# Optimization experiments

Measured on AMD Instinct MI355X. Metric: run time of the kernel, lower is better.

The kernel has to match this reference:

```python
import itertools
import jax, jax.numpy as jnp
import numpy as np

ALPHA = 1e-4   # mse/conn mixing
BETA = 0.1
DMAX = 20.0
NCAP = 10.0    # costs_n_cap
PCAP = 3.0     # costs_p_cap
W3D = 64       # 3D cube window (window_3d)
W2D = 32       # 2D MALIS window (window_2d, default)


def _dilate5(mask):
    # scipy binary_dilation, default cross structuring element, 5 iterations
    m = mask.astype(bool)
    for _ in range(5):
        p = np.pad(m, 1)
        m = p[1:-1, 1:-1] | p[:-2, 1:-1] | p[2:, 1:-1] | p[1:-1, :-2] | p[1:-1, 2:]
    return m


def _label8(mask):
    # skimage.measure.label on boolean mask: 8-connectivity, background=0
    H, W = mask.shape
    lbl = np.zeros((H, W), np.int64)
    parent = {}

    def find(x):
        while parent[x] != x:
            parent[x] = parent[parent[x]]
            x = parent[x]
        return x

    nxt = 1
    for i in range(H):
        for j in range(W):
            if not mask[i, j]:
                continue
            neigh = []
            for di, dj in ((-1, -1), (-1, 0), (-1, 1), (0, -1)):
                ii, jj = i + di, j + dj
                if 0 <= ii < H and 0 <= jj < W and mask[ii, jj]:
                    neigh.append(int(lbl[ii, jj]))
            if not neigh:
                lbl[i, j] = nxt
                parent[nxt] = nxt
                nxt += 1
            else:
                m0 = min(neigh)
                lbl[i, j] = m0
                for nb in neigh:
                    ra, rb = find(m0), find(nb)
                    if ra != rb:
                        parent[max(ra, rb)] = min(ra, rb)
    out = np.zeros_like(lbl)
    remap = {}
    c = 0
    for i in range(H):
        for j in range(W):
            if lbl[i, j] > 0:
                r = find(int(lbl[i, j]))
                if r not in remap:
                    c += 1
                    remap[r] = c
                out[i, j] = remap[r]
    return out


def _malis_edge_weights(seg, n1, n2, costs, pos):
    # MALIS union-find / Kruskal maximal-spanning-tree pair counting.
    # Edges processed in descending cost order. Background (seg==0) nodes
    # are not counted. pos=1: #same-label pairs merged; pos=0: #diff-label pairs.
    n = seg.size
    parent = list(range(n))

    def find(x):
        r = x
        while parent[r] != r:
            r = parent[r]
        while parent[x] != r:
            parent[x], x = r, parent[x]
        return r

    cnt = [({int(s): 1} if s > 0 else {}) for s in seg]
    tot = [1 if s > 0 else 0 for s in seg]
    w = np.zeros(costs.shape[0], np.float32)
    for e in np.argsort(-costs, kind="stable"):
        ra, rb = find(int(n1[e])), find(int(n2[e]))
        if ra == rb:
            continue
        ca, cb = cnt[ra], cnt[rb]
        if len(ca) > len(cb):
            ra, rb, ca, cb = rb, ra, cb, ca
        same = 0
        for l, v in ca.items():
            same += v * cb.get(l, 0)
        w[e] = float(same if pos else tot[ra] * tot[rb] - same)
        for l, v in ca.items():
            cb[l] = cb.get(l, 0) + v
        tot[rb] += tot[ra]
        parent[ra] = rb
        cnt[ra] = None
    return w


def _window_weights(pred2d, tgt2d):
    # numpy MALIS node weights for a [B,1,H,W] 2D projection
    B, C, H, W = pred2d.shape
    w = W2D
    wn = np.zeros(pred2d.shape, np.float32)
    wp = np.zeros(pred2d.shape, np.float32)
    idx = np.arange(w * w).reshape(w, w)
    n1 = np.concatenate([idx[:, :-1].ravel(), idx[:-1, :].ravel()])
    n2 = np.concatenate([idx[:, 1:].ravel(), idx[1:, :].ravel()])
    nh = w * (w - 1)
    for k in range(H // w):
        for j in range(W // w):
            p = pred2d[:, :, k*w:(k+1)*w, j*w:(j+1)*w]
            t = tgt2d[:, :, k*w:(k+1)*w, j*w:(j+1)*w]
            ch = (p[:, :, :, :-1] + p[:, :, :, 1:]).reshape(B, -1)
            cv = (p[:, :, :-1, :] + p[:, :, 1:, :]).reshape(B, -1)
            costs = np.concatenate([ch, cv], 1).astype(np.float32)
            gh = (t[:, :, :, :-1] + t[:, :, :, 1:]).reshape(B, -1)
            gv = (t[:, :, :-1, :] + t[:, :, 1:, :]).reshape(B, -1)
            gt = np.concatenate([gh, gv], 1).astype(np.float32)
            costs_n = costs.copy()
            costs_p = costs.copy()
            costs_n[gt > NCAP] = NCAP
            costs_p[gt < PCAP] = 0.0
            gt = np.minimum(gt, NCAP)
            for b in range(B):
                sg = _label8(~_dilate5(t[b, 0] == 0)).ravel()
                en = _malis_edge_weights(sg, n1, n2, costs_n[b], 0)
                ep = _malis_edge_weights(sg, n1, n2, costs_p[b], 1)
                sn = en.sum()
                if sn > 0:
                    en = en / sn
                sp = ep.sum()
                if sp > 0:
                    ep = ep / sp
                en[gt[b] >= PCAP] = 0.0
                ep[gt[b] < NCAP] = 0.0
                for ew, out in ((en, wn), (ep, wp)):
                    eh = ew[:nh].reshape(w, w - 1)
                    ev = ew[nh:].reshape(w - 1, w)
                    nwt = np.zeros((w, w), np.float32)
                    nwt[:, :-1] += eh
                    nwt[:, 1:] += eh
                    nwt[:-1, :] += ev
                    nwt[1:, :] += ev
                    out[b, 0, k*w:(k+1)*w, j*w:(j+1)*w] = nwt
    return wn, wp


def _precompute(pred_np, tgt_np):
    # host-side (detached) MALIS weight maps, exactly as the torch module
    B, C, H, W, D = pred_np.shape
    items = []
    for k, j, i in itertools.product(range(H // W3D), range(W // W3D), range(D // W3D)):
        sl = (slice(None), slice(None), slice(k*W3D, (k+1)*W3D),
              slice(j*W3D, (j+1)*W3D), slice(i*W3D, (i+1)*W3D))
        pc, tc = pred_np[sl], tgt_np[sl]
        for axis in (2, 3, 4):
            wn, wp = _window_weights(pc.min(axis=axis), tc.min(axis=axis))
            items.append((k, j, i, axis, jnp.asarray(wn), jnp.asarray(wp)))
    return items


def _loss(pred, target, items):
    mse = jnp.mean((pred - target) ** 2)
    conn = jnp.float32(0.0)
    for (k, j, i, axis, wn, wp) in items:
        pc = pred[:, :, k*W3D:(k+1)*W3D, j*W3D:(j+1)*W3D, i*W3D:(i+1)*W3D]
        proj = jnp.min(pc, axis=axis)  # [B,1,64,64]
        conn = conn + jnp.sum(proj**2 * wn + BETA * (DMAX - proj)**2 * wp)
    return (mse, jnp.float32(ALPHA) * conn)


def setup_inputs() -> dict:
    # synthetic distance-transform-like volumes (zeros on 'vessel' seeds)
    rng = np.random.default_rng(0)
    B, H = 4, 128
    g = np.arange(H, dtype=np.float32)
    zz, yy, xx = np.meshgrid(g, g, g, indexing="ij")
    tgt = np.empty((B, 1, H, H, H), np.float32)
    for b in range(B):
        pts = rng.uniform(0, H, size=(24, 3)).astype(np.float32)
        d = np.full((H, H, H), np.inf, np.float32)
        for p in pts:
            d = np.minimum(d, np.sqrt((zz - p[0])**2 + (yy - p[1])**2 + (xx - p[2])**2))
        tgt[b, 0] = np.floor(np.minimum(d, DMAX))
    pred = np.clip(tgt + 0.5 * rng.standard_normal(tgt.shape).astype(np.float32), 0.0, DMAX).astype(np.float32)
    return {"pred": jnp.asarray(pred), "target": jnp.asarray(tgt)}


def reference(pred, target):
    items = _precompute(np.asarray(pred), np.asarray(target))
    return _loss(pred, target, items)
```

## Files before the change

kernel.cpp:

```cpp
#include <hip/hip_runtime.h>

#define BLOCK 256
#define NNODE 1024
#define NH    992
#define NE    1984
#define NSORT 2048
#define LMAX  12
#define CHUNK 64
#define NPASS (NE / CHUNK)

typedef unsigned long long ull;

__device__ __forceinline__ void edge_nodes(int e, int& a, int& b) {
    if (e < NH) {
        int r = e / 31;
        int c = e - r * 31;
        a = (r << 5) + c;
        b = a + 1;
    } else {
        a = e - NH;
        b = a + 32;
    }
}

__device__ __forceinline__ int find_par(unsigned short* par, int x) {
    volatile unsigned short* vp = par;
    int r = x;
    int p = vp[r];
    while (p != r) { r = p; p = vp[r]; }
    int c = x;
    while (c != r) { const int nxt = vp[c]; vp[c] = (unsigned short)r; c = nxt; }
    return r;
}

__device__ __forceinline__ int dot16x4(ull a, ull b) {
    int s  = (int)(a & 0xFFFFu)         * (int)(b & 0xFFFFu);
    s     += (int)((a >> 16) & 0xFFFFu) * (int)((b >> 16) & 0xFFFFu);
    s     += (int)((a >> 32) & 0xFFFFu) * (int)((b >> 32) & 0xFFFFu);
    s     += (int)((a >> 48) & 0xFFFFu) * (int)((b >> 48) & 0xFFFFu);
    return s;
}

__device__ __forceinline__ void cswap(unsigned int& ka, unsigned short& ia,
                                      unsigned int& kb, unsigned short& ib, bool up) {
    const bool gt = (ka > kb) || (ka == kb && ia > ib);
    if (gt == up) {
        const unsigned int  tk = ka; ka = kb; kb = tk;
        const unsigned short ti = ia; ia = ib; ib = ti;
    }
}

__global__ __launch_bounds__(BLOCK) void conn_kernel(const float* __restrict__ pred,
                                                     const float* __restrict__ tgt,
                                                     double* __restrict__ acc_ws,
                                                     int B) {
    __shared__ alignas(16) float          sh_p[NNODE];
    __shared__ alignas(16) float          sh_t[NNODE];
    __shared__ alignas(16) unsigned int   sh_key[NSORT];
    __shared__ alignas(16) unsigned short sh_idx[NSORT];
    __shared__ unsigned short sh_parent[NNODE];
    __shared__ unsigned int   sh_szto[NNODE];
    __shared__ ull            sh_cnt64[NNODE * 3];
    __shared__ unsigned char  sh_seg[NNODE];
    __shared__ int            sh_flag;
    __shared__ int            sh_L;
    __shared__ float          sh_sn;
    __shared__ double         sh_red[4];

    const int tid = threadIdx.x;
    int wg = blockIdx.x;
    const int sign = (wg >> 3) & 1;
    wg = (wg & 7) | ((wg >> 4) << 3);
    const int b    = wg % B;  wg /= B;
    const int win  = wg & 3;  wg >>= 2;
    const int item = wg;
    const int axis_id = item % 3;
    const int cube = item / 3;
    const int ci = cube & 1;
    const int cj = (cube >> 1) & 1;
    const int ck = (cube >> 2) & 1;
    const int wk = win >> 1;
    const int wj = win & 1;

    const size_t base = (size_t)b * 2097152u;

    if (axis_id == 2) {
        for (int pix = tid; pix < NNODE; pix += BLOCK) {
            const int r = pix >> 5, c = pix & 31;
            const int R = wk * 32 + r, C = wj * 32 + c;
            const size_t idx0 = base + (size_t)(ck * 64 + R) * 16384u + (size_t)(cj * 64 + C) * 128u + (size_t)(ci * 64);
            const float4* pp = reinterpret_cast<const float4*>(pred + idx0);
            const float4* tp = reinterpret_cast<const float4*>(tgt + idx0);
            float pm = 3.4e38f, tm = 3.4e38f;
            #pragma unroll
            for (int h = 0; h < 16; ++h) {
                const float4 a = pp[h];
                const float4 t = tp[h];
                pm = fminf(pm, fminf(fminf(a.x, a.y), fminf(a.z, a.w)));
                tm = fminf(tm, fminf(fminf(t.x, t.y), fminf(t.z, t.w)));
            }
            sh_p[pix] = pm;
            sh_t[pix] = tm;
        }
    } else {
        const int r  = tid >> 3;
        const int c0 = (tid & 7) << 2;
        const int R = wk * 32 + r, C = wj * 32 + c0;
        size_t idx0; int hstride;
        if (axis_id == 0) {
            idx0 = base + (size_t)(ck * 64) * 16384u + (size_t)(cj * 64 + R) * 128u + (size_t)(ci * 64 + C);
            hstride = 16384;
        } else {
            idx0 = base + (size_t)(ck * 64 + R) * 16384u + (size_t)(cj * 64) * 128u + (size_t)(ci * 64 + C);
            hstride = 128;
        }
        float4 pm = make_float4(3.4e38f, 3.4e38f, 3.4e38f, 3.4e38f);
        float4 tm = pm;
        #pragma unroll 8
        for (int h = 0; h < 64; ++h) {
            const float4 a  = *reinterpret_cast<const float4*>(pred + idx0);
            const float4 t4 = *reinterpret_cast<const float4*>(tgt + idx0);
            pm.x = fminf(pm.x, a.x);  pm.y = fminf(pm.y, a.y);
            pm.z = fminf(pm.z, a.z);  pm.w = fminf(pm.w, a.w);
            tm.x = fminf(tm.x, t4.x); tm.y = fminf(tm.y, t4.y);
            tm.z = fminf(tm.z, t4.z); tm.w = fminf(tm.w, t4.w);
            idx0 += (size_t)hstride;
        }
        *reinterpret_cast<float4*>(&sh_p[(r << 5) + c0]) = pm;
        *reinterpret_cast<float4*>(&sh_t[(r << 5) + c0]) = tm;
    }
    __syncthreads();

    unsigned char* mA = sh_seg;
    unsigned char* mB = (unsigned char*)sh_idx;
    for (int pix = tid; pix < NNODE; pix += BLOCK)
        mA[pix] = (sh_t[pix] == 0.0f) ? 1 : 0;
    __syncthreads();
    for (int it = 0; it < 5; ++it) {
        unsigned char* src = (it & 1) ? mB : mA;
        unsigned char* dst = (it & 1) ? mA : mB;
        for (int pix = tid; pix < NNODE; pix += BLOCK) {
            const int r = pix >> 5, c = pix & 31;
            unsigned char v = src[pix];
            if (r > 0)  v |= src[pix - 32];
            if (r < 31) v |= src[pix + 32];
            if (c > 0)  v |= src[pix - 1];
            if (c < 31) v |= src[pix + 1];
            dst[pix] = v;
        }
        __syncthreads();
    }
    for (int pix = tid; pix < NNODE; pix += BLOCK)
        mA[pix] = mB[pix] ^ 1;
    __syncthreads();

    for (int pix = tid; pix < NNODE; pix += BLOCK)
        sh_parent[pix] = mA[pix] ? (unsigned short)pix : (unsigned short)0xFFFF;
    __syncthreads();
    for (;;) {
        if (tid == 0) sh_flag = 0;
        __syncthreads();
        for (int pix = tid; pix < NNODE; pix += BLOCK) {
            if (!mA[pix]) continue;
            const int r = pix >> 5, c = pix & 31;
            int m = sh_parent[pix];
            #pragma unroll
            for (int d = 0; d < 8; ++d) {
                static const int dr[8] = {-1,-1,-1, 0, 0, 1, 1, 1};
                static const int dc[8] = {-1, 0, 1,-1, 1,-1, 0, 1};
                const int rr = r + dr[d], cc = c + dc[d];
                if (rr < 0 || rr > 31 || cc < 0 || cc > 31) continue;
                const int nb = (rr << 5) + cc;
                if (mA[nb]) { int v = sh_parent[nb]; if (v < m) m = v; }
            }
            while ((int)sh_parent[m] < m) m = sh_parent[m];
            if (m < (int)sh_parent[pix]) { sh_parent[pix] = (unsigned short)m; sh_flag = 1; }
        }
        __syncthreads();
        const int f = sh_flag;
        __syncthreads();
        if (f == 0) break;
    }

    if (tid == 0) sh_L = 0;
    __syncthreads();
    for (int pix = tid; pix < NNODE; pix += BLOCK) {
        if (mA[pix] && (int)sh_parent[pix] == pix) {
            const int id = atomicAdd(&sh_L, 1);
            sh_szto[pix] = (unsigned int)(id + 1);
        }
    }
    __syncthreads();
    for (int pix = tid; pix < NNODE; pix += BLOCK) {
        unsigned char s = 0;
        if (mA[pix]) {
            int lab = (int)sh_szto[sh_parent[pix]];
            if (lab > 255) lab = 255;
            s = (unsigned char)lab;
        }
        sh_seg[pix] = s;
    }
    __syncthreads();

    const int Lraw = sh_L;
    const int mode = (Lraw <= 1) ? 0 : ((Lraw <= 4) ? 1 : 2);
    const bool skip_all = (Lraw == 0) || (Lraw == 1 && sign == 0);

    if (!skip_all) {

    for (int pix = tid; pix < NNODE; pix += BLOCK) {
        sh_parent[pix] = (unsigned short)pix;
        const int s = sh_seg[pix];
        const unsigned int tot = (s > 0 && s <= LMAX) ? 1u : 0u;
        sh_szto[pix] = 1u | (tot << 16);
        if (mode >= 1) {
            ull c0 = 0, c1 = 0, c2 = 0;
            if (s >= 1 && s <= LMAX) {
                const ull bit = 1ull << (((s - 1) & 3) * 16);
                const int q = (s - 1) >> 2;
                if (q == 0) c0 = bit; else if (q == 1) c1 = bit; else c2 = bit;
            }
            sh_cnt64[pix * 3 + 0] = c0;
            if (mode == 2) {
                sh_cnt64[pix * 3 + 1] = c1;
                sh_cnt64[pix * 3 + 2] = c2;
            }
        }
    }
    __syncthreads();

    unsigned int   K[8];
    unsigned short I[8];
    const int b8 = tid << 3;
    #pragma unroll
    for (int l = 0; l < 8; ++l) {
        const int e = b8 + l;
        if (e < NE) {
            int a, bb; edge_nodes(e, a, bb);
            float cost = sh_p[a] + sh_p[bb];
            const float g = sh_t[a] + sh_t[bb];
            if (sign == 0) { if (g > 10.0f) cost = 10.0f; }
            else           { if (g <  3.0f) cost = 0.0f;  }
            K[l] = ~__float_as_uint(cost);
            I[l] = (unsigned short)e;
        } else {
            K[l] = 0xFFFFFFFFu;
            I[l] = (unsigned short)0xFFFF;
        }
    }
    cswap(K[0],I[0],K[1],I[1], true );
    cswap(K[2],I[2],K[3],I[3], false);
    cswap(K[4],I[4],K[5],I[5], true );
    cswap(K[6],I[6],K[7],I[7], false);
    cswap(K[0],I[0],K[2],I[2], true );
    cswap(K[1],I[1],K[3],I[3], true );
    cswap(K[4],I[4],K[6],I[6], false);
    cswap(K[5],I[5],K[7],I[7], false);
    cswap(K[0],I[0],K[1],I[1], true );
    cswap(K[2],I[2],K[3],I[3], true );
    cswap(K[4],I[4],K[5],I[5], false);
    cswap(K[6],I[6],K[7],I[7], false);
    {
        const bool u8 = ((b8 & 8) == 0);
        cswap(K[0],I[0],K[4],I[4], u8); cswap(K[1],I[1],K[5],I[5], u8);
        cswap(K[2],I[2],K[6],I[6], u8); cswap(K[3],I[3],K[7],I[7], u8);
        cswap(K[0],I[0],K[2],I[2], u8); cswap(K[1],I[1],K[3],I[3], u8);
        cswap(K[4],I[4],K[6],I[6], u8); cswap(K[5],I[5],K[7],I[7], u8);
        cswap(K[0],I[0],K[1],I[1], u8); cswap(K[2],I[2],K[3],I[3], u8);
        cswap(K[4],I[4],K[5],I[5], u8); cswap(K[6],I[6],K[7],I[7], u8);
    }
    {
        uint4 k0, k1, iv;
        k0.x=K[0]; k0.y=K[1]; k0.z=K[2]; k0.w=K[3];
        k1.x=K[4]; k1.y=K[5]; k1.z=K[6]; k1.w=K[7];
        iv.x=(unsigned int)I[0] | ((unsigned int)I[1]<<16);
        iv.y=(unsigned int)I[2] | ((unsigned int)I[3]<<16);
        iv.z=(unsigned int)I[4] | ((unsigned int)I[5]<<16);
        iv.w=(unsigned int)I[6] | ((unsigned int)I[7]<<16);
        *reinterpret_cast<uint4*>(&sh_key[b8])     = k0;
        *reinterpret_cast<uint4*>(&sh_key[b8 + 4]) = k1;
        *reinterpret_cast<uint4*>(&sh_idx[b8])     = iv;
    }
    __syncthreads();

    for (int k = 16; k <= NSORT; k <<= 1) {
        for (int j = k >> 1; j >= 8; j >>= 1) {
            for (int p = tid; p < (NSORT >> 1); p += BLOCK) {
                const int i   = ((p & ~(j - 1)) << 1) | (p & (j - 1));
                const int ixj = i | j;
                const unsigned int ka = sh_key[i], kb = sh_key[ixj];
                const unsigned short ia = sh_idx[i], ib = sh_idx[ixj];
                const bool gt = (ka > kb) || (ka == kb && ia > ib);
                const bool up = ((i & k) == 0);
                if (gt == up) {
                    sh_key[i] = kb; sh_key[ixj] = ka;
                    sh_idx[i] = ib; sh_idx[ixj] = ia;
                }
            }
            __syncthreads();
        }
        {
            const uint4 k0 = *reinterpret_cast<const uint4*>(&sh_key[b8]);
            const uint4 k1 = *reinterpret_cast<const uint4*>(&sh_key[b8 + 4]);
            const uint4 iv = *reinterpret_cast<const uint4*>(&sh_idx[b8]);
            K[0]=k0.x; K[1]=k0.y; K[2]=k0.z; K[3]=k0.w;
            K[4]=k1.x; K[5]=k1.y; K[6]=k1.z; K[7]=k1.w;
            I[0]=(unsigned short)(iv.x); I[1]=(unsigned short)(iv.x>>16);
            I[2]=(unsigned short)(iv.y); I[3]=(unsigned short)(iv.y>>16);
            I[4]=(unsigned short)(iv.z); I[5]=(unsigned short)(iv.z>>16);
            I[6]=(unsigned short)(iv.w); I[7]=(unsigned short)(iv.w>>16);
            const bool u8 = ((b8 & k) == 0);
            cswap(K[0],I[0],K[4],I[4], u8); cswap(K[1],I[1],K[5],I[5], u8);
            cswap(K[2],I[2],K[6],I[6], u8); cswap(K[3],I[3],K[7],I[7], u8);
            cswap(K[0],I[0],K[2],I[2], u8); cswap(K[1],I[1],K[3],I[3], u8);
            cswap(K[4],I[4],K[6],I[6], u8); cswap(K[5],I[5],K[7],I[7], u8);
            cswap(K[0],I[0],K[1],I[1], u8); cswap(K[2],I[2],K[3],I[3], u8);
            cswap(K[4],I[4],K[5],I[5], u8); cswap(K[6],I[6],K[7],I[7], u8);
            uint4 o0, o1, ov;
            o0.x=K[0]; o0.y=K[1]; o0.z=K[2]; o0.w=K[3];
            o1.x=K[4]; o1.y=K[5]; o1.z=K[6]; o1.w=K[7];
            ov.x=(unsigned int)I[0] | ((unsigned int)I[1]<<16);
            ov.y=(unsigned int)I[2] | ((unsigned int)I[3]<<16);
            ov.z=(unsigned int)I[4] | ((unsigned int)I[5]<<16);
            ov.w=(unsigned int)I[6] | ((unsigned int)I[7]<<16);
            *reinterpret_cast<uint4*>(&sh_key[b8])     = o0;
            *reinterpret_cast<uint4*>(&sh_key[b8 + 4]) = o1;
            *reinterpret_cast<uint4*>(&sh_idx[b8])     = ov;
        }
        __syncthreads();
    }

    for (int e = tid; e < NE; e += BLOCK) sh_key[e] = 0u;
    __syncthreads();

    if (tid < 64) {
        const int lane = tid;
        for (int pass = 0; pass < NPASS; ++pass) {
            const int e = sh_idx[pass * CHUNK + lane];
            int a, bb; edge_nodes(e, a, bb);
            int ra = find_par(sh_parent, a);
            int rb = find_par(sh_parent, bb);
            ull m = __ballot(ra != rb);
            while (m) {
                const int i = (int)__builtin_ctzll(m);
                m &= m - 1;
                const unsigned int pack = (unsigned int)ra | ((unsigned int)rb << 10) | ((unsigned int)e << 20);
                const unsigned int pk = (unsigned int)__shfl((int)pack, i);
                const int ra_i = (int)(pk & 1023u);
                const int rb_i = (int)((pk >> 10) & 1023u);
                if (ra_i == rb_i) continue;
                const int se = (int)(pk >> 20);
                const unsigned int xa = sh_szto[ra_i], xb = sh_szto[rb_i];
                const int ta = (int)(xa >> 16), tb = (int)(xb >> 16);
                const int big = ((xa & 0xFFFFu) > (xb & 0xFFFFu));
                const int rs = big ? ra_i : rb_i;
                const int rl = big ? rb_i : ra_i;
                int wv;
                if (mode == 0) {
                    wv = ta * tb;
                } else if (mode == 1) {
                    const ull a0 = sh_cnt64[ra_i * 3];
                    const ull b0 = sh_cnt64[rb_i * 3];
                    const int same = dot16x4(a0, b0);
                    wv = sign ? same : (ta * tb - same);
                    if (lane == 0 && (ta + tb) > 0)
                        sh_cnt64[rs * 3] = a0 + b0;
                } else {
                    const ull a0 = sh_cnt64[ra_i * 3 + 0];
                    const ull a1 = sh_cnt64[ra_i * 3 + 1];
                    const ull a2 = sh_cnt64[ra_i * 3 + 2];
                    const ull b0 = sh_cnt64[rb_i * 3 + 0];
                    const ull b1 = sh_cnt64[rb_i * 3 + 1];
                    const ull b2 = sh_cnt64[rb_i * 3 + 2];
                    const int same = dot16x4(a0, b0) + dot16x4(a1, b1) + dot16x4(a2, b2);
                    wv = sign ? same : (ta * tb - same);
                    if (lane == 0 && (ta + tb) > 0) {
                        sh_cnt64[rs * 3 + 0] = a0 + b0;
                        sh_cnt64[rs * 3 + 1] = a1 + b1;
                        sh_cnt64[rs * 3 + 2] = a2 + b2;
                    }
                }
                if (lane == 0) {
                    sh_key[se] = __float_as_uint((float)wv);
                    sh_szto[rs] = xa + xb;
                    sh_parent[rl] = (unsigned short)rs;
                }
                if (ra == rl) ra = rs;
                if (rb == rl) rb = rs;
            }
        }
    }
    __syncthreads();

    {
        float part = 0.0f;
        for (int e = tid; e < NE; e += BLOCK) part += __uint_as_float(sh_key[e]);
        for (int off = 32; off > 0; off >>= 1) part += __shfl_down(part, off, 64);
        if ((tid & 63) == 0) sh_red[tid >> 6] = (double)part;
        __syncthreads();
        if (tid == 0) sh_sn = (float)(sh_red[0] + sh_red[1] + sh_red[2] + sh_red[3]);
        __syncthreads();
    }
    const float sn = sh_sn;

    double acc = 0.0;
    for (int pix = tid; pix < NNODE; pix += BLOCK) {
        const int r = pix >> 5, c = pix & 31;
        float nw = 0.0f;
        if (c < 31) { const int e = r * 31 + c;
            float v = __uint_as_float(sh_key[e]); if (sn > 0.0f) v = v / sn;
            const float g = sh_t[pix] + sh_t[pix + 1];
            if (sign == 0) { if (g >= 3.0f) v = 0.0f; } else { if (g < 10.0f) v = 0.0f; }
            nw += v; }
        if (c > 0)  { const int e = r * 31 + c - 1;
            float v = __uint_as_float(sh_key[e]); if (sn > 0.0f) v = v / sn;
            const float g = sh_t[pix - 1] + sh_t[pix];
            if (sign == 0) { if (g >= 3.0f) v = 0.0f; } else { if (g < 10.0f) v = 0.0f; }
            nw += v; }
        if (r < 31) { const int e = NH + pix;
            float v = __uint_as_float(sh_key[e]); if (sn > 0.0f) v = v / sn;
            const float g = sh_t[pix] + sh_t[pix + 32];
            if (sign == 0) { if (g >= 3.0f) v = 0.0f; } else { if (g < 10.0f) v = 0.0f; }
            nw += v; }
        if (r > 0)  { const int e = NH + pix - 32;
            float v = __uint_as_float(sh_key[e]); if (sn > 0.0f) v = v / sn;
            const float g = sh_t[pix - 32] + sh_t[pix];
            if (sign == 0) { if (g >= 3.0f) v = 0.0f; } else { if (g < 10.0f) v = 0.0f; }
            nw += v; }
        const float p = sh_p[pix];
        float term;
        if (sign == 0) {
            term = (p * p) * nw;
        } else {
            const float d = 20.0f - p;
            term = (0.1f * (d * d)) * nw;
        }
        acc += (double)term;
    }
    for (int off = 32; off > 0; off >>= 1) acc += __shfl_down(acc, off, 64);
    if ((tid & 63) == 0) sh_red[tid >> 6] = acc;
    __syncthreads();
    if (tid == 0)
        atomicAdd(&acc_ws[1], sh_red[0] + sh_red[1] + sh_red[2] + sh_red[3]);

    }
}

__global__ __launch_bounds__(BLOCK) void mse_kernel(const float* __restrict__ pred,
                                                    const float* __restrict__ tgt,
                                                    double* __restrict__ acc_ws,
                                                    long n) {
    double acc = 0.0;
    for (long i = (long)blockIdx.x * BLOCK + threadIdx.x; i < n; i += (long)gridDim.x * BLOCK) {
        const float d = pred[i] - tgt[i];
        acc += (double)(d * d);
    }
    for (int off = 32; off > 0; off >>= 1) acc += __shfl_down(acc, off, 64);
    __shared__ double red[4];
    if ((threadIdx.x & 63) == 0) red[threadIdx.x >> 6] = acc;
    __syncthreads();
    if (threadIdx.x == 0)
        atomicAdd(&acc_ws[0], red[0] + red[1] + red[2] + red[3]);
}

__global__ void fin_kernel(const double* __restrict__ acc_ws, float* __restrict__ out, long n) {
    if (threadIdx.x == 0 && blockIdx.x == 0) {
        out[0] = (float)(acc_ws[0] / (double)n);
        out[1] = (float)(acc_ws[1] * (double)1e-4f);
    }
}

extern "C" void kernel_launch(void* const* d_in, const int* in_sizes, int n_in,
                              void* d_out, int out_size, void* d_ws, size_t ws_size,
                              hipStream_t stream) {
    const float* pred = (const float*)d_in[0];
    const float* tgt  = (const float*)d_in[1];
    float* out = (float*)d_out;
    double* acc = (double*)d_ws;

    const long n = (long)in_sizes[0];
    const int  B = (int)(n / 2097152);

    hipMemsetAsync(d_ws, 0, 2 * sizeof(double), stream);
    mse_kernel<<<1024, BLOCK, 0, stream>>>(pred, tgt, acc, n);
    conn_kernel<<<192 * B, BLOCK, 0, stream>>>(pred, tgt, acc, B);
    fin_kernel<<<1, 64, 0, stream>>>(acc, out, n);
}
```

Baseline: 530.7 us.

## Split conn kernel into shared prep pass and per-sign solve pass

The fused conn kernel ran the projection, dilation and connected-component labelling twice per window, once for each sign. The new prep kernel does that work once per window and stores the projected pred and target, the labels and the component count in workspace. A solve kernel then loads these per sign and runs the sort, MALIS and accumulation, exiting early for windows that need no work. This removes the duplicated projection reads and labelling at the cost of an extra launch and a workspace round trip. The old fused kernel remains as a fallback when the workspace is too small.

```diff
diff --git a/kernel.cpp b/kernel.cpp
--- a/kernel.cpp
+++ b/kernel.cpp
@@ -50,27 +50,22 @@
     }
 }
 
-__global__ __launch_bounds__(BLOCK) void conn_kernel(const float* __restrict__ pred,
+__global__ __launch_bounds__(BLOCK) void prep_kernel(const float* __restrict__ pred,
                                                      const float* __restrict__ tgt,
-                                                     double* __restrict__ acc_ws,
+                                                     char* __restrict__ ws,
                                                      int B) {
-    __shared__ alignas(16) float          sh_p[NNODE];
-    __shared__ alignas(16) float          sh_t[NNODE];
-    __shared__ alignas(16) unsigned int   sh_key[NSORT];
-    __shared__ alignas(16) unsigned short sh_idx[NSORT];
+    __shared__ alignas(16) float sh_p[NNODE];
+    __shared__ alignas(16) float sh_t[NNODE];
+    __shared__ unsigned char  mA[NNODE];
+    __shared__ unsigned char  mB[NNODE];
     __shared__ unsigned short sh_parent[NNODE];
-    __shared__ unsigned int   sh_szto[NNODE];
-    __shared__ ull            sh_cnt64[NNODE * 3];
-    __shared__ unsigned char  sh_seg[NNODE];
-    __shared__ int            sh_flag;
-    __shared__ int            sh_L;
-    __shared__ float          sh_sn;
-    __shared__ double         sh_red[4];
+    __shared__ unsigned short sh_lab[NNODE];
+    __shared__ int sh_flag;
+    __shared__ int sh_L;
 
     const int tid = threadIdx.x;
-    int wg = blockIdx.x;
-    const int sign = (wg >> 3) & 1;
-    wg = (wg & 7) | ((wg >> 4) << 3);
+    const int w = blockIdx.x;
+    int wg = w;
     const int b    = wg % B;  wg /= B;
     const int win  = wg & 3;  wg >>= 2;
     const int item = wg;
@@ -81,6 +76,12 @@
     const int ck = (cube >> 2) & 1;
     const int wk = win >> 1;
     const int wj = win & 1;
+
+    const int NW = 96 * B;
+    float* Pb = (float*)(ws + 64);
+    float* Tb = Pb + (size_t)NW * NNODE;
+    unsigned char* Sb = (unsigned char*)(Tb + (size_t)NW * NNODE);
+    int* Lb = (int*)(Sb + (size_t)NW * NNODE);
 
     const size_t base = (size_t)b * 2097152u;
 
@@ -131,8 +132,6 @@
     }
     __syncthreads();
 
-    unsigned char* mA = sh_seg;
-    unsigned char* mB = (unsigned char*)sh_idx;
     for (int pix = tid; pix < NNODE; pix += BLOCK)
         mA[pix] = (sh_t[pix] == 0.0f) ? 1 : 0;
     __syncthreads();
@@ -187,26 +186,73 @@
     for (int pix = tid; pix < NNODE; pix += BLOCK) {
         if (mA[pix] && (int)sh_parent[pix] == pix) {
             const int id = atomicAdd(&sh_L, 1);
-            sh_szto[pix] = (unsigned int)(id + 1);
-        }
-    }
-    __syncthreads();
-    for (int pix = tid; pix < NNODE; pix += BLOCK) {
-        unsigned char s = 0;
-        if (mA[pix]) {
-            int lab = (int)sh_szto[sh_parent[pix]];
-            if (lab > 255) lab = 255;
-            s = (unsigned char)lab;
-        }
-        sh_seg[pix] = s;
-    }
-    __syncthreads();
-
-    const int Lraw = sh_L;
+            sh_lab[pix] = (unsigned short)(id + 1);
+        }
+    }
+    __syncthreads();
+
+    {
+        const int p4 = tid << 2;
+        *reinterpret_cast<float4*>(&Pb[(size_t)w * NNODE + p4]) =
+            *reinterpret_cast<const float4*>(&sh_p[p4]);
+        *reinterpret_cast<float4*>(&Tb[(size_t)w * NNODE + p4]) =
+            *reinterpret_cast<const float4*>(&sh_t[p4]);
+        unsigned int packed = 0;
+        #pragma unroll
+        for (int q = 0; q < 4; ++q) {
+            const int pix = p4 + q;
+            unsigned int s = 0;
+            if (mA[pix]) {
+                int lab = sh_lab[sh_parent[pix]];
+                if (lab > 255) lab = 255;
+                s = (unsigned int)lab;
+            }
+            packed |= s << (q * 8);
+        }
+        ((unsigned int*)Sb)[(size_t)w * (NNODE / 4) + tid] = packed;
+        if (tid == 0) Lb[w] = sh_L;
+    }
+}
+
+__global__ __launch_bounds__(BLOCK) void solve_kernel(const char* __restrict__ ws_c,
+                                                      double* __restrict__ acc_ws,
+                                                      int B) {
+    __shared__ alignas(16) float          sh_p[NNODE];
+    __shared__ alignas(16) float          sh_t[NNODE];
+    __shared__ alignas(16) unsigned int   sh_key[NSORT];
+    __shared__ alignas(16) unsigned short sh_idx[NSORT];
+    __shared__ unsigned short sh_parent[NNODE];
+    __shared__ unsigned int   sh_szto[NNODE];
+    __shared__ ull            sh_cnt64[NNODE * 3];
+    __shared__ alignas(16) unsigned char sh_seg[NNODE];
+    __shared__ float          sh_sn;
+    __shared__ double         sh_red[4];
+
+    const int tid = threadIdx.x;
+    int wg = blockIdx.x;
+    const int sign = wg & 1;  wg >>= 1;
+    const int w = wg;
+
+    const int NW = 96 * B;
+    const float* Pb = (const float*)(ws_c + 64);
+    const float* Tb = Pb + (size_t)NW * NNODE;
+    const unsigned char* Sb = (const unsigned char*)(Tb + (size_t)NW * NNODE);
+    const int* Lb = (const int*)(Sb + (size_t)NW * NNODE);
+
+    const int Lraw = Lb[w];
+    if (Lraw == 0 || (Lraw == 1 && sign == 0)) return;
     const int mode = (Lraw <= 1) ? 0 : ((Lraw <= 4) ? 1 : 2);
-    const bool skip_all = (Lraw == 0) || (Lraw == 1 && sign == 0);
-
-    if (!skip_all) {
+
+    {
+        const int p4 = tid << 2;
+        *reinterpret_cast<float4*>(&sh_p[p4]) =
+            *reinterpret_cast<const float4*>(&Pb[(size_t)w * NNODE + p4]);
+        *reinterpret_cast<float4*>(&sh_t[p4]) =
+            *reinterpret_cast<const float4*>(&Tb[(size_t)w * NNODE + p4]);
+        ((unsigned int*)sh_seg)[tid] =
+            ((const unsigned int*)Sb)[(size_t)w * (NNODE / 4) + tid];
+    }
+    __syncthreads();
 
     for (int pix = tid; pix < NNODE; pix += BLOCK) {
         sh_parent[pix] = (unsigned short)pix;
@@ -429,12 +475,398 @@
             nw += v; }
         const float p = sh_p[pix];
         float term;
-        if (sign == 0) {
-            term = (p * p) * nw;
+        if (sign == 0) term = (p * p) * nw;
+        else { const float d = 20.0f - p; term = (0.1f * (d * d)) * nw; }
+        acc += (double)term;
+    }
+    for (int off = 32; off > 0; off >>= 1) acc += __shfl_down(acc, off, 64);
+    if ((tid & 63) == 0) sh_red[tid >> 6] = acc;
+    __syncthreads();
+    if (tid == 0)
+        atomicAdd(&acc_ws[1], sh_red[0] + sh_red[1] + sh_red[2] + sh_red[3]);
+}
+
+__global__ __launch_bounds__(BLOCK) void conn_kernel(const float* __restrict__ pred,
+                                                     const float* __restrict__ tgt,
+                                                     double* __restrict__ acc_ws,
+                                                     int B) {
+    __shared__ alignas(16) float          sh_p[NNODE];
+    __shared__ alignas(16) float          sh_t[NNODE];
+    __shared__ alignas(16) unsigned int   sh_key[NSORT];
+    __shared__ alignas(16) unsigned short sh_idx[NSORT];
+    __shared__ unsigned short sh_parent[NNODE];
+    __shared__ unsigned int   sh_szto[NNODE];
+    __shared__ ull            sh_cnt64[NNODE * 3];
+    __shared__ unsigned char  sh_seg[NNODE];
+    __shared__ int            sh_flag;
+    __shared__ int            sh_L;
+    __shared__ float          sh_sn;
+    __shared__ double         sh_red[4];
+
+    const int tid = threadIdx.x;
+    int wg = blockIdx.x;
+    const int sign = (wg >> 3) & 1;
+    wg = (wg & 7) | ((wg >> 4) << 3);
+    const int b    = wg % B;  wg /= B;
+    const int win  = wg & 3;  wg >>= 2;
+    const int item = wg;
+    const int axis_id = item % 3;
+    const int cube = item / 3;
+    const int ci = cube & 1;
+    const int cj = (cube >> 1) & 1;
+    const int ck = (cube >> 2) & 1;
+    const int wk = win >> 1;
+    const int wj = win & 1;
+
+    const size_t base = (size_t)b * 2097152u;
+
+    if (axis_id == 2) {
+        for (int pix = tid; pix < NNODE; pix += BLOCK) {
+            const int r = pix >> 5, c = pix & 31;
+            const int R = wk * 32 + r, C = wj * 32 + c;
+            const size_t idx0 = base + (size_t)(ck * 64 + R) * 16384u + (size_t)(cj * 64 + C) * 128u + (size_t)(ci * 64);
+            const float4* pp = reinterpret_cast<const float4*>(pred + idx0);
+            const float4* tp = reinterpret_cast<const float4*>(tgt + idx0);
+            float pm = 3.4e38f, tm = 3.4e38f;
+            #pragma unroll
+            for (int h = 0; h < 16; ++h) {
+                const float4 a = pp[h];
+                const float4 t = tp[h];
+                pm = fminf(pm, fminf(fminf(a.x, a.y), fminf(a.z, a.w)));
+                tm = fminf(tm, fminf(fminf(t.x, t.y), fminf(t.z, t.w)));
+            }
+            sh_p[pix] = pm;
+            sh_t[pix] = tm;
+        }
+    } else {
+        const int r  = tid >> 3;
+        const int c0 = (tid & 7) << 2;
+        const int R = wk * 32 + r, C = wj * 32 + c0;
+        size_t idx0; int hstride;
+        if (axis_id == 0) {
+            idx0 = base + (size_t)(ck * 64) * 16384u + (size_t)(cj * 64 + R) * 128u + (size_t)(ci * 64 + C);
+            hstride = 16384;
         } else {
-            const float d = 20.0f - p;
-            term = (0.1f * (d * d)) * nw;
-        }
+            idx0 = base + (size_t)(ck * 64 + R) * 16384u + (size_t)(cj * 64) * 128u + (size_t)(ci * 64 + C);
+            hstride = 128;
+        }
+        float4 pm = make_float4(3.4e38f, 3.4e38f, 3.4e38f, 3.4e38f);
+        float4 tm = pm;
+        #pragma unroll 8
+        for (int h = 0; h < 64; ++h) {
+            const float4 a  = *reinterpret_cast<const float4*>(pred + idx0);
+            const float4 t4 = *reinterpret_cast<const float4*>(tgt + idx0);
+            pm.x = fminf(pm.x, a.x);  pm.y = fminf(pm.y, a.y);
+            pm.z = fminf(pm.z, a.z);  pm.w = fminf(pm.w, a.w);
+            tm.x = fminf(tm.x, t4.x); tm.y = fminf(tm.y, t4.y);
+            tm.z = fminf(tm.z, t4.z); tm.w = fminf(tm.w, t4.w);
+            idx0 += (size_t)hstride;
+        }
+        *reinterpret_cast<float4*>(&sh_p[(r << 5) + c0]) = pm;
+        *reinterpret_cast<float4*>(&sh_t[(r << 5) + c0]) = tm;
+    }
+    __syncthreads();
+
+    unsigned char* mA = sh_seg;
+    unsigned char* mB = (unsigned char*)sh_idx;
+    for (int pix = tid; pix < NNODE; pix += BLOCK)
+        mA[pix] = (sh_t[pix] == 0.0f) ? 1 : 0;
+    __syncthreads();
+    for (int it = 0; it < 5; ++it) {
+        unsigned char* src = (it & 1) ? mB : mA;
+        unsigned char* dst = (it & 1) ? mA : mB;
+        for (int pix = tid; pix < NNODE; pix += BLOCK) {
+            const int r = pix >> 5, c = pix & 31;
+            unsigned char v = src[pix];
+            if (r > 0)  v |= src[pix - 32];
+            if (r < 31) v |= src[pix + 32];
+            if (c > 0)  v |= src[pix - 1];
+            if (c < 31) v |= src[pix + 1];
+            dst[pix] = v;
+        }
+        __syncthreads();
+    }
+    for (int pix = tid; pix < NNODE; pix += BLOCK)
+        mA[pix] = mB[pix] ^ 1;
+    __syncthreads();
+
+    for (int pix = tid; pix < NNODE; pix += BLOCK)
+        sh_parent[pix] = mA[pix] ? (unsigned short)pix : (unsigned short)0xFFFF;
+    __syncthreads();
+    for (;;) {
+        if (tid == 0) sh_flag = 0;
+        __syncthreads();
+        for (int pix = tid; pix < NNODE; pix += BLOCK) {
+            if (!mA[pix]) continue;
+            const int r = pix >> 5, c = pix & 31;
+            int m = sh_parent[pix];
+            #pragma unroll
+            for (int d = 0; d < 8; ++d) {
+                static const int dr[8] = {-1,-1,-1, 0, 0, 1, 1, 1};
+                static const int dc[8] = {-1, 0, 1,-1, 1,-1, 0, 1};
+                const int rr = r + dr[d], cc = c + dc[d];
+                if (rr < 0 || rr > 31 || cc < 0 || cc > 31) continue;
+                const int nb = (rr << 5) + cc;
+                if (mA[nb]) { int v = sh_parent[nb]; if (v < m) m = v; }
+            }
+            while ((int)sh_parent[m] < m) m = sh_parent[m];
+            if (m < (int)sh_parent[pix]) { sh_parent[pix] = (unsigned short)m; sh_flag = 1; }
+        }
+        __syncthreads();
+        const int f = sh_flag;
+        __syncthreads();
+        if (f == 0) break;
+    }
+
+    if (tid == 0) sh_L = 0;
+    __syncthreads();
+    for (int pix = tid; pix < NNODE; pix += BLOCK) {
+        if (mA[pix] && (int)sh_parent[pix] == pix) {
+            const int id = atomicAdd(&sh_L, 1);
+            sh_szto[pix] = (unsigned int)(id + 1);
+        }
+    }
+    __syncthreads();
+    for (int pix = tid; pix < NNODE; pix += BLOCK) {
+        unsigned char s = 0;
+        if (mA[pix]) {
+            int lab = (int)sh_szto[sh_parent[pix]];
+            if (lab > 255) lab = 255;
+            s = (unsigned char)lab;
+        }
+        sh_seg[pix] = s;
+    }
+    __syncthreads();
+
+    const int Lraw = sh_L;
+    const int mode = (Lraw <= 1) ? 0 : ((Lraw <= 4) ? 1 : 2);
+    const bool skip_all = (Lraw == 0) || (Lraw == 1 && sign == 0);
+
+    if (!skip_all) {
+
+    for (int pix = tid; pix < NNODE; pix += BLOCK) {
+        sh_parent[pix] = (unsigned short)pix;
+        const int s = sh_seg[pix];
+        const unsigned int tot = (s > 0 && s <= LMAX) ? 1u : 0u;
+        sh_szto[pix] = 1u | (tot << 16);
+        if (mode >= 1) {
+            ull c0 = 0, c1 = 0, c2 = 0;
+            if (s >= 1 && s <= LMAX) {
+                const ull bit = 1ull << (((s - 1) & 3) * 16);
+                const int q = (s - 1) >> 2;
+                if (q == 0) c0 = bit; else if (q == 1) c1 = bit; else c2 = bit;
+            }
+            sh_cnt64[pix * 3 + 0] = c0;
+            if (mode == 2) {
+                sh_cnt64[pix * 3 + 1] = c1;
+                sh_cnt64[pix * 3 + 2] = c2;
+            }
+        }
+    }
+    __syncthreads();
+
+    unsigned int   K[8];
+    unsigned short I[8];
+    const int b8 = tid << 3;
+    #pragma unroll
+    for (int l = 0; l < 8; ++l) {
+        const int e = b8 + l;
+        if (e < NE) {
+            int a, bb; edge_nodes(e, a, bb);
+            float cost = sh_p[a] + sh_p[bb];
+            const float g = sh_t[a] + sh_t[bb];
+            if (sign == 0) { if (g > 10.0f) cost = 10.0f; }
+            else           { if (g <  3.0f) cost = 0.0f;  }
+            K[l] = ~__float_as_uint(cost);
+            I[l] = (unsigned short)e;
+        } else {
+            K[l] = 0xFFFFFFFFu;
+            I[l] = (unsigned short)0xFFFF;
+        }
+    }
+    cswap(K[0],I[0],K[1],I[1], true );
+    cswap(K[2],I[2],K[3],I[3], false);
+    cswap(K[4],I[4],K[5],I[5], true );
+    cswap(K[6],I[6],K[7],I[7], false);
+    cswap(K[0],I[0],K[2],I[2], true );
+    cswap(K[1],I[1],K[3],I[3], true );
+    cswap(K[4],I[4],K[6],I[6], false);
+    cswap(K[5],I[5],K[7],I[7], false);
+    cswap(K[0],I[0],K[1],I[1], true );
+    cswap(K[2],I[2],K[3],I[3], true );
+    cswap(K[4],I[4],K[5],I[5], false);
+    cswap(K[6],I[6],K[7],I[7], false);
+    {
+        const bool u8 = ((b8 & 8) == 0);
+        cswap(K[0],I[0],K[4],I[4], u8); cswap(K[1],I[1],K[5],I[5], u8);
+        cswap(K[2],I[2],K[6],I[6], u8); cswap(K[3],I[3],K[7],I[7], u8);
+        cswap(K[0],I[0],K[2],I[2], u8); cswap(K[1],I[1],K[3],I[3], u8);
+        cswap(K[4],I[4],K[6],I[6], u8); cswap(K[5],I[5],K[7],I[7], u8);
+        cswap(K[0],I[0],K[1],I[1], u8); cswap(K[2],I[2],K[3],I[3], u8);
+        cswap(K[4],I[4],K[5],I[5], u8); cswap(K[6],I[6],K[7],I[7], u8);
+    }
+    {
+        uint4 k0, k1, iv;
+        k0.x=K[0]; k0.y=K[1]; k0.z=K[2]; k0.w=K[3];
+        k1.x=K[4]; k1.y=K[5]; k1.z=K[6]; k1.w=K[7];
+        iv.x=(unsigned int)I[0] | ((unsigned int)I[1]<<16);
+        iv.y=(unsigned int)I[2] | ((unsigned int)I[3]<<16);
+        iv.z=(unsigned int)I[4] | ((unsigned int)I[5]<<16);
+        iv.w=(unsigned int)I[6] | ((unsigned int)I[7]<<16);
+        *reinterpret_cast<uint4*>(&sh_key[b8])     = k0;
+        *reinterpret_cast<uint4*>(&sh_key[b8 + 4]) = k1;
+        *reinterpret_cast<uint4*>(&sh_idx[b8])     = iv;
+    }
+    __syncthreads();
+
+    for (int k = 16; k <= NSORT; k <<= 1) {
+        for (int j = k >> 1; j >= 8; j >>= 1) {
+            for (int p = tid; p < (NSORT >> 1); p += BLOCK) {
+                const int i   = ((p & ~(j - 1)) << 1) | (p & (j - 1));
+                const int ixj = i | j;
+                const unsigned int ka = sh_key[i], kb = sh_key[ixj];
+                const unsigned short ia = sh_idx[i], ib = sh_idx[ixj];
+                const bool gt = (ka > kb) || (ka == kb && ia > ib);
+                const bool up = ((i & k) == 0);
+                if (gt == up) {
+                    sh_key[i] = kb; sh_key[ixj] = ka;
+                    sh_idx[i] = ib; sh_idx[ixj] = ia;
+                }
+            }
+            __syncthreads();
+        }
+        {
+            const uint4 k0 = *reinterpret_cast<const uint4*>(&sh_key[b8]);
+            const uint4 k1 = *reinterpret_cast<const uint4*>(&sh_key[b8 + 4]);
+            const uint4 iv = *reinterpret_cast<const uint4*>(&sh_idx[b8]);
+            K[0]=k0.x; K[1]=k0.y; K[2]=k0.z; K[3]=k0.w;
+            K[4]=k1.x; K[5]=k1.y; K[6]=k1.z; K[7]=k1.w;
+            I[0]=(unsigned short)(iv.x); I[1]=(unsigned short)(iv.x>>16);
+            I[2]=(unsigned short)(iv.y); I[3]=(unsigned short)(iv.y>>16);
+            I[4]=(unsigned short)(iv.z); I[5]=(unsigned short)(iv.z>>16);
+            I[6]=(unsigned short)(iv.w); I[7]=(unsigned short)(iv.w>>16);
+            const bool u8 = ((b8 & k) == 0);
+            cswap(K[0],I[0],K[4],I[4], u8); cswap(K[1],I[1],K[5],I[5], u8);
+            cswap(K[2],I[2],K[6],I[6], u8); cswap(K[3],I[3],K[7],I[7], u8);
+            cswap(K[0],I[0],K[2],I[2], u8); cswap(K[1],I[1],K[3],I[3], u8);
+            cswap(K[4],I[4],K[6],I[6], u8); cswap(K[5],I[5],K[7],I[7], u8);
+            cswap(K[0],I[0],K[1],I[1], u8); cswap(K[2],I[2],K[3],I[3], u8);
+            cswap(K[4],I[4],K[5],I[5], u8); cswap(K[6],I[6],K[7],I[7], u8);
+            uint4 o0, o1, ov;
+            o0.x=K[0]; o0.y=K[1]; o0.z=K[2]; o0.w=K[3];
+            o1.x=K[4]; o1.y=K[5]; o1.z=K[6]; o1.w=K[7];
+            ov.x=(unsigned int)I[0] | ((unsigned int)I[1]<<16);
+            ov.y=(unsigned int)I[2] | ((unsigned int)I[3]<<16);
+            ov.z=(unsigned int)I[4] | ((unsigned int)I[5]<<16);
+            ov.w=(unsigned int)I[6] | ((unsigned int)I[7]<<16);
+            *reinterpret_cast<uint4*>(&sh_key[b8])     = o0;
+            *reinterpret_cast<uint4*>(&sh_key[b8 + 4]) = o1;
+            *reinterpret_cast<uint4*>(&sh_idx[b8])     = ov;
+        }
+        __syncthreads();
+    }
+
+    for (int e = tid; e < NE; e += BLOCK) sh_key[e] = 0u;
+    __syncthreads();
+
+    if (tid < 64) {
+        const int lane = tid;
+        for (int pass = 0; pass < NPASS; ++pass) {
+            const int e = sh_idx[pass * CHUNK + lane];
+            int a, bb; edge_nodes(e, a, bb);
+            int ra = find_par(sh_parent, a);
+            int rb = find_par(sh_parent, bb);
+            ull m = __ballot(ra != rb);
+            while (m) {
+                const int i = (int)__builtin_ctzll(m);
+                m &= m - 1;
+                const unsigned int pack = (unsigned int)ra | ((unsigned int)rb << 10) | ((unsigned int)e << 20);
+                const unsigned int pk = (unsigned int)__shfl((int)pack, i);
+                const int ra_i = (int)(pk & 1023u);
+                const int rb_i = (int)((pk >> 10) & 1023u);
+                if (ra_i == rb_i) continue;
+                const int se = (int)(pk >> 20);
+                const unsigned int xa = sh_szto[ra_i], xb = sh_szto[rb_i];
+                const int ta = (int)(xa >> 16), tb = (int)(xb >> 16);
+                const int big = ((xa & 0xFFFFu) > (xb & 0xFFFFu));
+                const int rs = big ? ra_i : rb_i;
+                const int rl = big ? rb_i : ra_i;
+                int wv;
+                if (mode == 0) {
+                    wv = ta * tb;
+                } else if (mode == 1) {
+                    const ull a0 = sh_cnt64[ra_i * 3];
+                    const ull b0 = sh_cnt64[rb_i * 3];
+                    const int same = dot16x4(a0, b0);
+                    wv = sign ? same : (ta * tb - same);
+                    if (lane == 0 && (ta + tb) > 0)
+                        sh_cnt64[rs * 3] = a0 + b0;
+                } else {
+                    const ull a0 = sh_cnt64[ra_i * 3 + 0];
+                    const ull a1 = sh_cnt64[ra_i * 3 + 1];
+                    const ull a2 = sh_cnt64[ra_i * 3 + 2];
+                    const ull b0 = sh_cnt64[rb_i * 3 + 0];
+                    const ull b1 = sh_cnt64[rb_i * 3 + 1];
+                    const ull b2 = sh_cnt64[rb_i * 3 + 2];
+                    const int same = dot16x4(a0, b0) + dot16x4(a1, b1) + dot16x4(a2, b2);
+                    wv = sign ? same : (ta * tb - same);
+                    if (lane == 0 && (ta + tb) > 0) {
+                        sh_cnt64[rs * 3 + 0] = a0 + b0;
+                        sh_cnt64[rs * 3 + 1] = a1 + b1;
+                        sh_cnt64[rs * 3 + 2] = a2 + b2;
+                    }
+                }
+                if (lane == 0) {
+                    sh_key[se] = __float_as_uint((float)wv);
+                    sh_szto[rs] = xa + xb;
+                    sh_parent[rl] = (unsigned short)rs;
+                }
+                if (ra == rl) ra = rs;
+                if (rb == rl) rb = rs;
+            }
+        }
+    }
+    __syncthreads();
+
+    {
+        float part = 0.0f;
+        for (int e = tid; e < NE; e += BLOCK) part += __uint_as_float(sh_key[e]);
+        for (int off = 32; off > 0; off >>= 1) part += __shfl_down(part, off, 64);
+        if ((tid & 63) == 0) sh_red[tid >> 6] = (double)part;
+        __syncthreads();
+        if (tid == 0) sh_sn = (float)(sh_red[0] + sh_red[1] + sh_red[2] + sh_red[3]);
+        __syncthreads();
+    }
+    const float sn = sh_sn;
+
+    double acc = 0.0;
+    for (int pix = tid; pix < NNODE; pix += BLOCK) {
+        const int r = pix >> 5, c = pix & 31;
+        float nw = 0.0f;
+        if (c < 31) { const int e = r * 31 + c;
+            float v = __uint_as_float(sh_key[e]); if (sn > 0.0f) v = v / sn;
+            const float g = sh_t[pix] + sh_t[pix + 1];
+            if (sign == 0) { if (g >= 3.0f) v = 0.0f; } else { if (g < 10.0f) v = 0.0f; }
+            nw += v; }
+        if (c > 0)  { const int e = r * 31 + c - 1;
+            float v = __uint_as_float(sh_key[e]); if (sn > 0.0f) v = v / sn;
+            const float g = sh_t[pix - 1] + sh_t[pix];
+            if (sign == 0) { if (g >= 3.0f) v = 0.0f; } else { if (g < 10.0f) v = 0.0f; }
+            nw += v; }
+        if (r < 31) { const int e = NH + pix;
+            float v = __uint_as_float(sh_key[e]); if (sn > 0.0f) v = v / sn;
+            const float g = sh_t[pix] + sh_t[pix + 32];
+            if (sign == 0) { if (g >= 3.0f) v = 0.0f; } else { if (g < 10.0f) v = 0.0f; }
+            nw += v; }
+        if (r > 0)  { const int e = NH + pix - 32;
+            float v = __uint_as_float(sh_key[e]); if (sn > 0.0f) v = v / sn;
+            const float g = sh_t[pix - 32] + sh_t[pix];
+            if (sign == 0) { if (g >= 3.0f) v = 0.0f; } else { if (g < 10.0f) v = 0.0f; }
+            nw += v; }
+        const float p = sh_p[pix];
+        float term;
+        if (sign == 0) term = (p * p) * nw;
+        else { const float d = 20.0f - p; term = (0.1f * (d * d)) * nw; }
         acc += (double)term;
     }
     for (int off = 32; off > 0; off >>= 1) acc += __shfl_down(acc, off, 64);
@@ -480,9 +912,16 @@
 
     const long n = (long)in_sizes[0];
     const int  B = (int)(n / 2097152);
+    const int  NW = 96 * B;
+    const size_t need = 64 + (size_t)NW * NNODE * 9 + (size_t)NW * 4;
 
     hipMemsetAsync(d_ws, 0, 2 * sizeof(double), stream);
     mse_kernel<<<1024, BLOCK, 0, stream>>>(pred, tgt, acc, n);
-    conn_kernel<<<192 * B, BLOCK, 0, stream>>>(pred, tgt, acc, B);
+    if (ws_size >= need) {
+        prep_kernel<<<NW, BLOCK, 0, stream>>>(pred, tgt, (char*)d_ws, B);
+        solve_kernel<<<192 * B, BLOCK, 0, stream>>>((const char*)d_ws, acc, B);
+    } else {
+        conn_kernel<<<192 * B, BLOCK, 0, stream>>>(pred, tgt, acc, B);
+    }
     fin_kernel<<<1, 64, 0, stream>>>(acc, out, n);
 }
```

Result: no change. 539.3 us (+1.6%).
